# Kernel optimization log

Hardware: AMD Instinct MI355X
Metric: run time of the kernel (lower is better)

## Reference

```python
import jax, jax.numpy as jnp
import numpy as np

E = 256  # embedding_dim

def setup_inputs() -> dict:
    key = jax.random.key(0)
    k1, k2, k3 = jax.random.split(key, 3)
    B, P, N, D = 32, 4, 1024, E
    x = jax.random.normal(k1, (B, P, N, D), dtype=jnp.float32)
    W_qkv = jax.random.normal(k2, (D, 1 + 2 * E), dtype=jnp.float32) * (1.0 / np.sqrt(D))
    b_qkv = jnp.zeros((1 + 2 * E,), dtype=jnp.float32)
    W_o = jax.random.normal(k3, (E, E), dtype=jnp.float32) * (1.0 / np.sqrt(E))
    b_o = jnp.zeros((E,), dtype=jnp.float32)
    return {"x": x, "W_qkv": W_qkv, "b_qkv": b_qkv, "W_o": W_o, "b_o": b_o}

def reference(x, W_qkv, b_qkv, W_o, b_o):
    # qkv projection: [B,P,N,D] @ [D,1+2E] -> [B,P,N,1+2E]
    qkv = jnp.einsum('bpnd,de->bpne', x, W_qkv) + b_qkv
    q = qkv[..., :1]                 # [B,P,N,1]
    k = qkv[..., 1:1 + E]            # [B,P,N,E]
    v = jax.nn.relu(qkv[..., 1 + E:])  # [B,P,N,E]
    # softmax over patch axis N (axis=2)
    context_scores = jax.nn.softmax(q, axis=2)
    # context vector: sum over N of k * scores -> [B,P,1,E]
    context_vector = jnp.sum(k * context_scores, axis=2, keepdims=True)
    # broadcast-multiply with relu(v): [B,P,N,E] * [B,P,1,E]
    updated_values = v * context_vector
    # output projection
    out = jnp.einsum('bpnd,de->bpne', updated_values, W_o) + b_o
    return out
```

## Files before the change

### kernel.cpp

```cpp
#include <hip/hip_runtime.h>
#include <hip/hip_bf16.h>

typedef float f32x4 __attribute__((ext_vector_type(4)));
typedef short s16x8 __attribute__((ext_vector_type(8)));
typedef __bf16 bf16x8 __attribute__((ext_vector_type(8)));
typedef unsigned short u16;

#define NSEQ 1024
#define EDIM 256

#define WAITVM(N) asm volatile("s_waitcnt vmcnt(" #N ")" ::: "memory")

__device__ __forceinline__ u16 f2bf(float f){
  union { float f; unsigned u; } v; v.f = f;
  unsigned r = v.u + 0x7FFF + ((v.u >> 16) & 1);
  return (u16)(r >> 16);
}
__device__ __forceinline__ float bf2f(u16 b){
  union { float f; unsigned u; } v; v.u = ((unsigned)b) << 16;
  return v.f;
}

template <typename V>
__device__ __forceinline__ auto mfma_impl(V a, V b, f32x4 c, int)
    -> decltype(__builtin_amdgcn_mfma_f32_16x16x32_bf16(a, b, c, 0, 0, 0)) {
  return __builtin_amdgcn_mfma_f32_16x16x32_bf16(a, b, c, 0, 0, 0);
}
template <typename V>
__device__ __forceinline__ f32x4 mfma_impl(V a, V b, f32x4 c, long){
  bf16x8 ab = __builtin_bit_cast(bf16x8, a);
  bf16x8 bb = __builtin_bit_cast(bf16x8, b);
  return __builtin_amdgcn_mfma_f32_16x16x32_bf16(ab, bb, c, 0, 0, 0);
}
__device__ __forceinline__ f32x4 mfma16(s16x8 a, s16x8 b, f32x4 c){
  return mfma_impl(a, b, c, 0);
}

__device__ __forceinline__ void gload_lds16(const u16* g, u16* l){
  __builtin_amdgcn_global_load_lds((const __attribute__((address_space(1))) void*)g,
                                   (__attribute__((address_space(3))) void*)l, 16, 0, 0);
}

__global__ void k0_prep(const float* __restrict__ Wqkv, const float* __restrict__ Wo,
                        u16* __restrict__ wvf, u16* __restrict__ wof, float* __restrict__ wqc){
  int t = blockIdx.x * 256 + threadIdx.x;
  if (t < 16384){
    int which = t >> 13;
    int slot  = t & 8191;
    int l  = slot & 63;
    int nt = (slot >> 6) & 1;
    int ks = (slot >> 7) & 7;
    int c  = (slot >> 10) & 7;
    int row = ks*32 + 8*(l>>4);
    int col = c*32 + nt*16 + (l&15);
    s16x8 o8;
    if (which == 0){
      for (int j=0;j<8;j++) o8[j] = (short)f2bf(Wqkv[(size_t)(row+j)*513 + 257 + col]);
      *(s16x8*)(wvf + (size_t)slot*8) = o8;
    } else {
      for (int j=0;j<8;j++) o8[j] = (short)f2bf(Wo[(size_t)(row+j)*256 + col]);
      *(s16x8*)(wof + (size_t)slot*8) = o8;
    }
  } else if (t < 16384 + 256){
    int d = t - 16384;
    wqc[d] = Wqkv[(size_t)d*513];
  }
}

__global__ void k1_qfrag(const float* __restrict__ x, const float* __restrict__ wqc,
                         const float* __restrict__ bqkv, u16* __restrict__ xf, float* __restrict__ q){
  int bp = blockIdx.x >> 6, rt = blockIdx.x & 63;
  const float* xt = x + ((size_t)bp*NSEQ + rt*16) * EDIM;
  __shared__ float xl[16][260];
  int tid = threadIdx.x;
  for (int i=0;i<4;i++){
    int idx = tid + i*256;
    float4 vv = ((const float4*)xt)[idx];
    int row = idx >> 6, c4 = idx & 63;
    *(float4*)&xl[row][c4*4] = vv;
  }
  __syncthreads();
  int l = tid & 63, w = tid >> 6;
  int lo = l & 15, hi = l >> 4;
  for (int kk=0;kk<2;kk++){
    int ks = w*2 + kk;
    int k0 = ks*32 + 8*hi;
    s16x8 o8;
    for (int j=0;j<8;j++) o8[j] = (short)f2bf(xl[lo][k0+j]);
    size_t fo = ((((size_t)bp*64 + rt)*8 + ks)*64 + l) * 8;
    *(s16x8*)(xf + fo) = o8;
  }
  int c = l*4;
  float4 wv4 = *(const float4*)(wqc + c);
  float b0 = bqkv[0];
  for (int r=0;r<4;r++){
    int row = w*4 + r;
    float4 xv = *(float4*)&xl[row][c];
    float p = xv.x*wv4.x + xv.y*wv4.y + xv.z*wv4.z + xv.w*wv4.w;
    for (int o=32;o;o>>=1) p += __shfl_down(p, o);
    if (l == 0) q[(size_t)bp*NSEQ + rt*16 + row] = p + b0;
  }
}

__global__ void k2_softmax(const float* __restrict__ q, float* __restrict__ s){
  int bp = blockIdx.x, tid = threadIdx.x;
  float4 v = ((const float4*)(q + (size_t)bp*NSEQ))[tid];
  __shared__ float red[8];
  float m = fmaxf(fmaxf(v.x, v.y), fmaxf(v.z, v.w));
  for (int o=32;o;o>>=1) m = fmaxf(m, __shfl_xor(m, o));
  if ((tid & 63) == 0) red[tid >> 6] = m;
  __syncthreads();
  m = fmaxf(fmaxf(red[0], red[1]), fmaxf(red[2], red[3]));
  float e0 = expf(v.x - m), e1 = expf(v.y - m), e2 = expf(v.z - m), e3 = expf(v.w - m);
  float sum = e0 + e1 + e2 + e3;
  for (int o=32;o;o>>=1) sum += __shfl_xor(sum, o);
  if ((tid & 63) == 0) red[4 + (tid >> 6)] = sum;
  __syncthreads();
  float inv = 1.0f / (red[4] + red[5] + red[6] + red[7]);
  float4 o4 = {e0*inv, e1*inv, e2*inv, e3*inv};
  ((float4*)(s + (size_t)bp*NSEQ))[tid] = o4;
}

__global__ void k3_tpart(const u16* __restrict__ xf, const float* __restrict__ s, float* __restrict__ tp){
  int bp = blockIdx.x >> 3, ks = blockIdx.x & 7;
  int tid = threadIdx.x, l = tid & 63, w = tid >> 6;
  int lo = l & 15, hi = l >> 4;
  const float* sb = s + (size_t)bp*NSEQ;
  float acc[8];
  for (int j=0;j<8;j++) acc[j] = 0.f;
  for (int rti=0; rti<16; rti++){
    int rt = w*16 + rti;
    s16x8 v = *(const s16x8*)(xf + ((((size_t)bp*64 + rt)*8 + ks)*64 + l)*8);
    float sv = sb[rt*16 + lo];
    for (int j=0;j<8;j++) acc[j] += sv * bf2f((u16)v[j]);
  }
  for (int j=0;j<8;j++)
    for (int m=1;m<16;m<<=1) acc[j] += __shfl_xor(acc[j], m);
  __shared__ float red[4][32];
  if (lo == 0)
    for (int j=0;j<8;j++) red[w][8*hi + j] = acc[j];
  __syncthreads();
  if (tid < 32){
    float t = red[0][tid] + red[1][tid] + red[2][tid] + red[3][tid];
    tp[(size_t)bp*EDIM + ks*32 + tid] = t;
  }
}

__global__ void k4_cv(const float* __restrict__ tp, const float* __restrict__ Wqkv,
                      const float* __restrict__ bqkv, float* __restrict__ cv){
  int bp = blockIdx.x, e = threadIdx.x;
  __shared__ float tl[256];
  tl[e] = tp[(size_t)bp*EDIM + e];
  __syncthreads();
  float acc = bqkv[1 + e];
  for (int d=0;d<256;d++) acc += tl[d] * Wqkv[(size_t)d*513 + 1 + e];
  cv[(size_t)bp*EDIM + e] = acc;
}

__global__ __launch_bounds__(256, 2) void k5_main(
    const u16* __restrict__ xf, const u16* __restrict__ wvf, const u16* __restrict__ wof,
    const float* __restrict__ bqkv, const float* __restrict__ bo,
    const float* __restrict__ cv, float* __restrict__ out){
  int bp = blockIdx.x >> 3, rt = blockIdx.x & 7;
  int tid = threadIdx.x, l = tid & 63, w = tid >> 6;
  int lo = l & 15, hi = l >> 4;
  __shared__ u16 WBUF[3][16][512];
  __shared__ u16 HB[4][2][16][40];

  s16x8 af0[8], af1[8];
  {
    const u16* src0 = xf + ((((size_t)bp*64 + rt*8 + 2*w + 0)*8)*64 + l)*8;
    const u16* src1 = src0 + 4096;
#pragma unroll
    for (int ks=0;ks<8;ks++){
      af0[ks] = *(const s16x8*)(src0 + (size_t)ks*512);
      af1[ks] = *(const s16x8*)(src1 + (size_t)ks*512);
    }
  }
  const float* cvb = cv + (size_t)bp*EDIM;
  float* ob0 = out + ((size_t)bp*NSEQ + (rt*8 + 2*w + 0)*16) * EDIM;
  float* ob1 = ob0 + 16*EDIM;

  auto stage = [&](int chunk, int buf){
    const u16* base = (chunk < 8) ? (wvf + (size_t)chunk*8192) : (wof + (size_t)(chunk-8)*8192);
    const u16* gsrc = base + (size_t)(w*4)*512 + l*8;
#pragma unroll
    for (int i=0;i<4;i++) gload_lds16(gsrc + i*512, &WBUF[buf][w*4 + i][0]);
  };

  stage(0, 0);
  stage(1, 1);
  WAITVM(4);
  __builtin_amdgcn_s_barrier();
  __builtin_amdgcn_sched_barrier(0);

  s16x8 hf0[8], hf1[8];

#pragma unroll
  for (int c=0;c<16;c++){
    const int buf = c % 3;
    f32x4 acc00 = {0.f,0.f,0.f,0.f}, acc01 = acc00, acc10 = acc00, acc11 = acc00;
    auto do_mfma = [&](const s16x8 (&A0)[8], const s16x8 (&A1)[8]){
#pragma unroll
      for (int ks=0;ks<8;ks++){
        s16x8 b0 = *(const s16x8*)&WBUF[buf][ks*2 + 0][l*8];
        s16x8 b1 = *(const s16x8*)&WBUF[buf][ks*2 + 1][l*8];
        acc00 = mfma16(A0[ks], b0, acc00);
        acc10 = mfma16(A1[ks], b0, acc10);
        acc01 = mfma16(A0[ks], b1, acc01);
        acc11 = mfma16(A1[ks], b1, acc11);
      }
    };
    if (c < 8) do_mfma(af0, af1); else do_mfma(hf0, hf1);

    if (c < 8){
      int colA = c*32 + lo, colB = colA + 16;
      float bvA = bqkv[257 + colA], bvB = bqkv[257 + colB];
      float csA = cvb[colA],        csB = cvb[colB];
#pragma unroll
      for (int r=0;r<4;r++){
        float h00 = acc00[r] + bvA, h01 = acc01[r] + bvB;
        float h10 = acc10[r] + bvA, h11 = acc11[r] + bvB;
        HB[w][0][hi*4 + r][lo]      = f2bf(h00 > 0.f ? h00*csA : 0.f);
        HB[w][0][hi*4 + r][16 + lo] = f2bf(h01 > 0.f ? h01*csB : 0.f);
        HB[w][1][hi*4 + r][lo]      = f2bf(h10 > 0.f ? h10*csA : 0.f);
        HB[w][1][hi*4 + r][16 + lo] = f2bf(h11 > 0.f ? h11*csB : 0.f);
      }
      hf0[c] = *(const s16x8*)&HB[w][0][lo][8*hi];
      hf1[c] = *(const s16x8*)&HB[w][1][lo][8*hi];
    } else {
      int c2 = c - 8;
      int colA = c2*32 + lo, colB = colA + 16;
      float bbA = bo[colA], bbB = bo[colB];
#pragma unroll
      for (int r=0;r<4;r++){
        ob0[(size_t)(hi*4 + r)*EDIM + colA] = acc00[r] + bbA;
        ob0[(size_t)(hi*4 + r)*EDIM + colB] = acc01[r] + bbB;
        ob1[(size_t)(hi*4 + r)*EDIM + colA] = acc10[r] + bbA;
        ob1[(size_t)(hi*4 + r)*EDIM + colB] = acc11[r] + bbB;
      }
    }

    if (c + 2 <= 15) stage(c + 2, (c + 2) % 3);

    if (c < 8)       WAITVM(4);
    else if (c < 14) WAITVM(20);
    else if (c == 14) WAITVM(16);
    if (c < 15){
      __builtin_amdgcn_s_barrier();
      __builtin_amdgcn_sched_barrier(0);
    }
  }
}

extern "C" void kernel_launch(void* const* d_in, const int* in_sizes, int n_in,
                              void* d_out, int out_size, void* d_ws, size_t ws_size,
                              hipStream_t stream){
  const float* x    = (const float*)d_in[0];
  const float* Wqkv = (const float*)d_in[1];
  const float* bqkv = (const float*)d_in[2];
  const float* Wo   = (const float*)d_in[3];
  const float* bo   = (const float*)d_in[4];
  float* out = (float*)d_out;
  char* ws = (char*)d_ws;
  u16*   xf  = (u16*)(ws);
  u16*   wvf = (u16*)(ws + 67108864);
  u16*   wof = (u16*)(ws + 67239936);
  float* q   = (float*)(ws + 67371008);
  float* s   = (float*)(ws + 67895296);
  float* tp  = (float*)(ws + 68419584);
  float* cvv = (float*)(ws + 69468160);
  float* wqc = (float*)(ws + 69599232);

  hipLaunchKernelGGL(k0_prep,    dim3(65),   dim3(256), 0, stream, Wqkv, Wo, wvf, wof, wqc);
  hipLaunchKernelGGL(k1_qfrag,   dim3(8192), dim3(256), 0, stream, x, wqc, bqkv, xf, q);
  hipLaunchKernelGGL(k2_softmax, dim3(128),  dim3(256), 0, stream, q, s);
  hipLaunchKernelGGL(k3_tpart,   dim3(1024), dim3(256), 0, stream, xf, s, tp);
  hipLaunchKernelGGL(k4_cv,      dim3(128),  dim3(256), 0, stream, tp, Wqkv, bqkv, cvv);
  hipLaunchKernelGGL(k5_main,    dim3(1024), dim3(256), 0, stream, xf, wvf, wof, bqkv, bo, cvv, out);
}
```

Baseline: 130.1 us.

## Fuse softmax, weighted reduction and context projection into one kernel; prioritize MFMA waves

Merges the softmax, score-weighted x reduction and context-vector projection into a single kernel with one 512-thread block per (b,p). This removes two launches and the global round trips for the scores and partial sums. It also raises wave priority around the MFMA loop in the main kernel. The trade-off is parallelism: the x reduction now runs on 128 blocks instead of 1024, so each block streams 64 tiles serially, which may leave much of the GPU idle during that phase.

```diff
diff --git a/kernel.cpp b/kernel.cpp
--- a/kernel.cpp
+++ b/kernel.cpp
@@ -102,59 +102,66 @@
   }
 }
 
-__global__ void k2_softmax(const float* __restrict__ q, float* __restrict__ s){
-  int bp = blockIdx.x, tid = threadIdx.x;
-  float4 v = ((const float4*)(q + (size_t)bp*NSEQ))[tid];
-  __shared__ float red[8];
-  float m = fmaxf(fmaxf(v.x, v.y), fmaxf(v.z, v.w));
-  for (int o=32;o;o>>=1) m = fmaxf(m, __shfl_xor(m, o));
-  if ((tid & 63) == 0) red[tid >> 6] = m;
-  __syncthreads();
-  m = fmaxf(fmaxf(red[0], red[1]), fmaxf(red[2], red[3]));
-  float e0 = expf(v.x - m), e1 = expf(v.y - m), e2 = expf(v.z - m), e3 = expf(v.w - m);
-  float sum = e0 + e1 + e2 + e3;
-  for (int o=32;o;o>>=1) sum += __shfl_xor(sum, o);
-  if ((tid & 63) == 0) red[4 + (tid >> 6)] = sum;
-  __syncthreads();
-  float inv = 1.0f / (red[4] + red[5] + red[6] + red[7]);
-  float4 o4 = {e0*inv, e1*inv, e2*inv, e3*inv};
-  ((float4*)(s + (size_t)bp*NSEQ))[tid] = o4;
-}
-
-__global__ void k3_tpart(const u16* __restrict__ xf, const float* __restrict__ s, float* __restrict__ tp){
-  int bp = blockIdx.x >> 3, ks = blockIdx.x & 7;
+__global__ __launch_bounds__(512) void k234(
+    const u16* __restrict__ xf, const float* __restrict__ q,
+    const float* __restrict__ Wqkv, const float* __restrict__ bqkv,
+    float* __restrict__ cv){
+  int bp = blockIdx.x;
   int tid = threadIdx.x, l = tid & 63, w = tid >> 6;
   int lo = l & 15, hi = l >> 4;
-  const float* sb = s + (size_t)bp*NSEQ;
+  __shared__ float sm[1024];
+  __shared__ float red[16];
+  __shared__ float tl[256];
+  __shared__ float cvp[2][256];
+
+  float2 v = ((const float2*)(q + (size_t)bp*NSEQ))[tid];
+  float m = fmaxf(v.x, v.y);
+  for (int o=32;o;o>>=1) m = fmaxf(m, __shfl_xor(m, o));
+  if (l == 0) red[w] = m;
+  __syncthreads();
+  m = red[0];
+#pragma unroll
+  for (int i=1;i<8;i++) m = fmaxf(m, red[i]);
+  float e0 = expf(v.x - m), e1 = expf(v.y - m);
+  float ss = e0 + e1;
+  for (int o=32;o;o>>=1) ss += __shfl_xor(ss, o);
+  if (l == 0) red[8 + w] = ss;
+  __syncthreads();
+  float tot = red[8];
+#pragma unroll
+  for (int i=1;i<8;i++) tot += red[8 + i];
+  float inv = 1.0f / tot;
+  sm[2*tid]   = e0 * inv;
+  sm[2*tid+1] = e1 * inv;
+  __syncthreads();
+
   float acc[8];
+#pragma unroll
   for (int j=0;j<8;j++) acc[j] = 0.f;
-  for (int rti=0; rti<16; rti++){
-    int rt = w*16 + rti;
-    s16x8 v = *(const s16x8*)(xf + ((((size_t)bp*64 + rt)*8 + ks)*64 + l)*8);
-    float sv = sb[rt*16 + lo];
-    for (int j=0;j<8;j++) acc[j] += sv * bf2f((u16)v[j]);
-  }
+  const u16* base = xf + (((size_t)bp*64)*8 + w)*512 + (size_t)l*8;
+  for (int rt=0; rt<64; rt++){
+    s16x8 d8 = *(const s16x8*)(base + (size_t)rt*4096);
+    float sv = sm[rt*16 + lo];
+#pragma unroll
+    for (int j=0;j<8;j++) acc[j] += sv * bf2f((u16)d8[j]);
+  }
+#pragma unroll
   for (int j=0;j<8;j++)
-    for (int m=1;m<16;m<<=1) acc[j] += __shfl_xor(acc[j], m);
-  __shared__ float red[4][32];
-  if (lo == 0)
-    for (int j=0;j<8;j++) red[w][8*hi + j] = acc[j];
-  __syncthreads();
-  if (tid < 32){
-    float t = red[0][tid] + red[1][tid] + red[2][tid] + red[3][tid];
-    tp[(size_t)bp*EDIM + ks*32 + tid] = t;
-  }
-}
-
-__global__ void k4_cv(const float* __restrict__ tp, const float* __restrict__ Wqkv,
-                      const float* __restrict__ bqkv, float* __restrict__ cv){
-  int bp = blockIdx.x, e = threadIdx.x;
-  __shared__ float tl[256];
-  tl[e] = tp[(size_t)bp*EDIM + e];
-  __syncthreads();
-  float acc = bqkv[1 + e];
-  for (int d=0;d<256;d++) acc += tl[d] * Wqkv[(size_t)d*513 + 1 + e];
-  cv[(size_t)bp*EDIM + e] = acc;
+    for (int mm=1;mm<16;mm<<=1) acc[j] += __shfl_xor(acc[j], mm);
+  if (lo == 0){
+#pragma unroll
+    for (int j=0;j<8;j++) tl[w*32 + 8*hi + j] = acc[j];
+  }
+  __syncthreads();
+
+  int e = tid & 255, half = tid >> 8;
+  float a = 0.f;
+  for (int d = half*128; d < half*128 + 128; d++)
+    a += tl[d] * Wqkv[(size_t)d*513 + 1 + e];
+  cvp[half][e] = a;
+  __syncthreads();
+  if (tid < 256)
+    cv[(size_t)bp*EDIM + tid] = bqkv[1 + tid] + cvp[0][tid] + cvp[1][tid];
 }
 
 __global__ __launch_bounds__(256, 2) void k5_main(
@@ -201,6 +208,7 @@
     const int buf = c % 3;
     f32x4 acc00 = {0.f,0.f,0.f,0.f}, acc01 = acc00, acc10 = acc00, acc11 = acc00;
     auto do_mfma = [&](const s16x8 (&A0)[8], const s16x8 (&A1)[8]){
+      __builtin_amdgcn_s_setprio(1);
 #pragma unroll
       for (int ks=0;ks<8;ks++){
         s16x8 b0 = *(const s16x8*)&WBUF[buf][ks*2 + 0][l*8];
@@ -210,6 +218,7 @@
         acc01 = mfma16(A0[ks], b1, acc01);
         acc11 = mfma16(A1[ks], b1, acc11);
       }
+      __builtin_amdgcn_s_setprio(0);
     };
     if (c < 8) do_mfma(af0, af1); else do_mfma(hf0, hf1);
 
@@ -267,15 +276,11 @@
   u16*   wvf = (u16*)(ws + 67108864);
   u16*   wof = (u16*)(ws + 67239936);
   float* q   = (float*)(ws + 67371008);
-  float* s   = (float*)(ws + 67895296);
-  float* tp  = (float*)(ws + 68419584);
   float* cvv = (float*)(ws + 69468160);
   float* wqc = (float*)(ws + 69599232);
 
   hipLaunchKernelGGL(k0_prep,    dim3(65),   dim3(256), 0, stream, Wqkv, Wo, wvf, wof, wqc);
   hipLaunchKernelGGL(k1_qfrag,   dim3(8192), dim3(256), 0, stream, x, wqc, bqkv, xf, q);
-  hipLaunchKernelGGL(k2_softmax, dim3(128),  dim3(256), 0, stream, q, s);
-  hipLaunchKernelGGL(k3_tpart,   dim3(1024), dim3(256), 0, stream, xf, s, tp);
-  hipLaunchKernelGGL(k4_cv,      dim3(128),  dim3(256), 0, stream, tp, Wqkv, bqkv, cvv);
+  hipLaunchKernelGGL(k234,       dim3(128),  dim3(512), 0, stream, xf, q, Wqkv, bqkv, cvv);
   hipLaunchKernelGGL(k5_main,    dim3(1024), dim3(256), 0, stream, xf, wvf, wof, bqkv, bo, cvv, out);
 }
```

Result: faster. 124.6 us (-4.2%).
